# Kernel tuning notes

Hardware: AMD Instinct MI355X
Metric: run time of the kernel (lower is better)

## Reference

```python
import jax, jax.numpy as jnp
import numpy as np

B, S, D, H = 2, 48, 256, 8
DH = D // H  # depth per head = 32
N = S * S    # flattened pair sequence length = 2304


def setup_inputs() -> dict:
    key = jax.random.key(0)
    ks = jax.random.split(key, 9)
    std = 1.0 / np.sqrt(D)
    x = jax.random.normal(ks[0], (B, S, S, D), dtype=jnp.float32)
    Wq = jax.random.normal(ks[1], (D, D), dtype=jnp.float32) * std
    Wk = jax.random.normal(ks[2], (D, D), dtype=jnp.float32) * std
    Wv = jax.random.normal(ks[3], (D, D), dtype=jnp.float32) * std
    Wo = jax.random.normal(ks[4], (D, D), dtype=jnp.float32) * std
    bq = jnp.zeros((D,), jnp.float32)
    bk = jnp.zeros((D,), jnp.float32)
    bv = jnp.zeros((D,), jnp.float32)
    bo = jnp.zeros((D,), jnp.float32)
    return {"pair_representation": x, "Wq": Wq, "bq": bq, "Wk": Wk, "bk": bk,
            "Wv": Wv, "bv": bv, "Wo": Wo, "bo": bo}


def reference(pair_representation, Wq, bq, Wk, bk, Wv, bv, Wo, bo):
    x = pair_representation.reshape(B, N, D)  # flatten (S,S) -> N

    def heads(t):  # (B,N,D) -> (B,H,N,DH)
        return t.reshape(B, N, H, DH).transpose(0, 2, 1, 3)

    q = heads(x @ Wq + bq)
    k = heads(x @ Wk + bk)
    v = heads(x @ Wv + bv)

    scale = 1.0 / jnp.sqrt(jnp.asarray(DH, jnp.float32))
    logits = jnp.einsum('bhnd,bhmd->bhnm', q, k) * scale  # (B,H,N,N)
    attn = jax.nn.softmax(logits, axis=-1)
    ctx = jnp.einsum('bhnm,bhmd->bhnd', attn, v)
    ctx = ctx.transpose(0, 2, 1, 3).reshape(B, N, D)
    return ctx @ Wo + bo  # (B, N, D)
```

## Files before the change

### kernel.cpp

```cpp
#include <hip/hip_runtime.h>
#include <math.h>

#define B 2
#define S 48
#define D 256
#define H 8
#define DH 32
#define N (S*S)
#define BN (B*N)
#define BH (B*H)
#define KS 6
#define KPZ (N/KS)
#define NE ((size_t)BN*D)
#define BHN (BH*N)

typedef _Float16 half8 __attribute__((ext_vector_type(8)));
typedef _Float16 half4_t __attribute__((ext_vector_type(4)));
typedef unsigned short ushort8_t __attribute__((ext_vector_type(8)));
typedef float floatx4 __attribute__((ext_vector_type(4)));

__device__ __forceinline__ half8 cvt8(const float* v) {
    half8 h;
    #pragma unroll
    for (int j = 0; j < 8; j++) h[j] = (_Float16)v[j];
    return h;
}

__global__ __launch_bounds__(256) void proj_kernel(
    const float* __restrict__ x,
    const float* __restrict__ Wq, const float* __restrict__ bq,
    const float* __restrict__ Wk, const float* __restrict__ bk,
    const float* __restrict__ Wv, const float* __restrict__ bv,
    _Float16* __restrict__ qbuf, _Float16* __restrict__ kbuf,
    _Float16* __restrict__ vtbuf)
{
    __shared__ __align__(16) _Float16 BhS[64 * 72];

    const int z = blockIdx.z;
    const float* W    = (z == 0) ? Wq : (z == 1) ? Wk : Wv;
    const float* bias = (z == 0) ? bq : (z == 1) ? bk : bv;
    const float scale = (z == 0) ? rsqrtf((float)DH) * 1.44269504f : 1.0f;

    const int t = threadIdx.x;
    const int wv2 = t >> 6, lane = t & 63, l15 = lane & 15, quad = lane >> 4;
    const int rowb = blockIdx.x * 64;
    const int colb = blockIdx.y * 64;
    const int grow = rowb + wv2 * 16 + l15;
    floatx4 acc[4] = {{0,0,0,0},{0,0,0,0},{0,0,0,0},{0,0,0,0}};

    for (int kb0 = 0; kb0 < D; kb0 += 64) {
        __syncthreads();
        #pragma unroll
        for (int i = 0; i < 2; i++) {
            int u = i * 256 + t;
            int cc = u & 63, k0 = (u >> 6) * 8;
            float v[8];
            #pragma unroll
            for (int j = 0; j < 8; j++)
                v[j] = W[(size_t)(kb0 + k0 + j) * D + colb + cc];
            *(half8*)(BhS + cc * 72 + k0) = cvt8(v);
        }
        __syncthreads();
        #pragma unroll
        for (int ksx = 0; ksx < 2; ksx++) {
            const float* xp = x + (size_t)grow * D + kb0 + ksx * 32 + quad * 8;
            float4 x0 = *(const float4*)xp;
            float4 x1 = *(const float4*)(xp + 4);
            float v[8] = {x0.x, x0.y, x0.z, x0.w, x1.x, x1.y, x1.z, x1.w};
            half8 ah = cvt8(v);
            #pragma unroll
            for (int cg = 0; cg < 4; cg++) {
                half8 bh8 = *(const half8*)(BhS + (cg * 16 + l15) * 72 + ksx * 32 + quad * 8);
                acc[cg] = __builtin_amdgcn_mfma_f32_16x16x32_f16(ah, bh8, acc[cg], 0, 0, 0);
            }
        }
    }

    const int bb = (rowb >= N) ? 1 : 0;
    #pragma unroll
    for (int cg = 0; cg < 4; cg++) {
        int col = colb + cg * 16 + l15;
        int hh = col >> 5, dh = col & 31;
        float bs = bias[col];
        if (z < 2) {
            _Float16* op = (z == 0) ? qbuf : kbuf;
            #pragma unroll
            for (int r = 0; r < 4; r++) {
                int n = rowb + wv2 * 16 + quad * 4 + r - bb * N;
                float v = (acc[cg][r] + bs) * scale;
                op[((size_t)(bb * H + hh) * N + n) * DH + dh] = (_Float16)v;
            }
        } else {
            int n0 = rowb + wv2 * 16 + quad * 4 - bb * N;
            half4_t pk;
            #pragma unroll
            for (int r = 0; r < 4; r++) pk[r] = (_Float16)(acc[cg][r] + bs);
            *(half4_t*)(vtbuf + ((size_t)(bb * H + hh) * DH + dh) * N + n0) = pk;
        }
    }
}

__global__ __launch_bounds__(256) void attn_kernel(
    const _Float16* __restrict__ qbuf, const _Float16* __restrict__ kbuf,
    const _Float16* __restrict__ vtbuf,
    _Float16* __restrict__ ctx_part, float* __restrict__ lpart)
{
    __shared__ __align__(16) _Float16 Ks[64 * 40];
    __shared__ __align__(16) _Float16 Vt[32 * 72];

    const int t = threadIdx.x;
    const int wv2 = t >> 6, lane = t & 63, l15 = lane & 15, quad = lane >> 4;
    const int bh = blockIdx.y, kz = blockIdx.z;
    const int qbase = blockIdx.x * 128 + wv2 * 32;

    half8 bq8[2];
    #pragma unroll
    for (int qg = 0; qg < 2; qg++)
        bq8[qg] = *(const half8*)(qbuf +
            ((size_t)bh * N + qbase + qg * 16 + l15) * DH + quad * 8);

    floatx4 acc[2][2] = {{{0,0,0,0},{0,0,0,0}},{{0,0,0,0},{0,0,0,0}}};
    float lsum[2] = {0.f, 0.f};

    const int skey = t >> 2, sd0 = (t & 3) * 8;
    const int svd = t >> 3, svk = (t & 7) * 8;

    for (int it = 0; it < KPZ / 64; it++) {
        const int key0 = kz * KPZ + it * 64;
        __syncthreads();
        *(ushort8_t*)(Ks + skey * 40 + sd0) =
            *(const ushort8_t*)(kbuf + ((size_t)bh * N + key0 + skey) * DH + sd0);
        *(ushort8_t*)(Vt + svd * 72 + svk) =
            *(const ushort8_t*)(vtbuf + ((size_t)bh * DH + svd) * N + key0 + svk);
        __syncthreads();

        #pragma unroll
        for (int kg = 0; kg < 4; kg++) {
            half8 ka = *(const half8*)(Ks + (kg * 16 + l15) * 40 + quad * 8);
            half4_t va0 = *(const half4_t*)(Vt + l15 * 72 + kg * 16 + quad * 4);
            half4_t va1 = *(const half4_t*)(Vt + (16 + l15) * 72 + kg * 16 + quad * 4);
            #pragma unroll
            for (int qg = 0; qg < 2; qg++) {
                floatx4 s = {0, 0, 0, 0};
                s = __builtin_amdgcn_mfma_f32_16x16x32_f16(ka, bq8[qg], s, 0, 0, 0);
                half4_t pf;
                #pragma unroll
                for (int r = 0; r < 4; r++) {
                    float p = exp2f(s[r]);
                    lsum[qg] += p;
                    pf[r] = (_Float16)p;
                }
                acc[qg][0] = __builtin_amdgcn_mfma_f32_16x16x16f16(va0, pf, acc[qg][0], 0, 0, 0);
                acc[qg][1] = __builtin_amdgcn_mfma_f32_16x16x16f16(va1, pf, acc[qg][1], 0, 0, 0);
            }
        }
    }

    const int bb = bh >> 3, hh = bh & 7;
    #pragma unroll
    for (int qg = 0; qg < 2; qg++) {
        float ls = lsum[qg];
        ls += __shfl_xor(ls, 16);
        ls += __shfl_xor(ls, 32);
        int q = qbase + qg * 16 + l15;
        if (quad == 0) lpart[(size_t)kz * BHN + bh * N + q] = ls;
        _Float16* crow = ctx_part + (size_t)kz * NE + ((size_t)bb * N + q) * D + hh * DH;
        half4_t c0, c1;
        #pragma unroll
        for (int r = 0; r < 4; r++) {
            c0[r] = (_Float16)acc[qg][0][r];
            c1[r] = (_Float16)acc[qg][1][r];
        }
        *(half4_t*)(crow + quad * 4)      = c0;
        *(half4_t*)(crow + 16 + quad * 4) = c1;
    }
}

__global__ __launch_bounds__(256) void outproj_kernel(
    const _Float16* __restrict__ ctx_part, const float* __restrict__ lpart,
    const float* __restrict__ Wo, const float* __restrict__ bo,
    float* __restrict__ out)
{
    __shared__ __align__(16) _Float16 BhS[64 * 72];
    __shared__ float Linv[64 * 8];

    const int t = threadIdx.x;
    const int wv2 = t >> 6, lane = t & 63, l15 = lane & 15, quad = lane >> 4;
    const int rowb = blockIdx.x * 64;
    const int colb = blockIdx.y * 64;
    const int grow = rowb + wv2 * 16 + l15;

    #pragma unroll
    for (int i = 0; i < 2; i++) {
        int idx = i * 256 + t;
        int r = idx >> 3, hh = idx & 7;
        int row = rowb + r;
        int bb = (row >= N) ? 1 : 0;
        int bhn = (bb * H + hh) * N + (row - bb * N);
        float ls = 0.f;
        #pragma unroll
        for (int zz = 0; zz < KS; zz++) ls += lpart[(size_t)zz * BHN + bhn];
        Linv[idx] = 1.0f / ls;
    }

    floatx4 acc[4] = {{0,0,0,0},{0,0,0,0},{0,0,0,0},{0,0,0,0}};

    for (int kb0 = 0; kb0 < D; kb0 += 64) {
        __syncthreads();
        #pragma unroll
        for (int i = 0; i < 2; i++) {
            int u = i * 256 + t;
            int cc = u & 63, k0 = (u >> 6) * 8;
            float v[8];
            #pragma unroll
            for (int j = 0; j < 8; j++)
                v[j] = Wo[(size_t)(kb0 + k0 + j) * D + colb + cc];
            *(half8*)(BhS + cc * 72 + k0) = cvt8(v);
        }
        __syncthreads();
        #pragma unroll
        for (int ksx = 0; ksx < 2; ksx++) {
            const int kcol = kb0 + ksx * 32 + quad * 8;
            float linv = Linv[(wv2 * 16 + l15) * 8 + (kcol >> 5)];
            float v[8] = {};
            #pragma unroll
            for (int zz = 0; zz < KS; zz++) {
                half8 h = *(const half8*)(ctx_part + (size_t)zz * NE + (size_t)grow * D + kcol);
                #pragma unroll
                for (int j = 0; j < 8; j++) v[j] += (float)h[j];
            }
            #pragma unroll
            for (int j = 0; j < 8; j++) v[j] *= linv;
            half8 ah = cvt8(v);
            #pragma unroll
            for (int cg = 0; cg < 4; cg++) {
                half8 bh8 = *(const half8*)(BhS + (cg * 16 + l15) * 72 + ksx * 32 + quad * 8);
                acc[cg] = __builtin_amdgcn_mfma_f32_16x16x32_f16(ah, bh8, acc[cg], 0, 0, 0);
            }
        }
    }

    #pragma unroll
    for (int cg = 0; cg < 4; cg++) {
        int col = colb + cg * 16 + l15;
        float bs = bo[col];
        #pragma unroll
        for (int r = 0; r < 4; r++) {
            int row = rowb + wv2 * 16 + quad * 4 + r;
            out[(size_t)row * D + col] = acc[cg][r] + bs;
        }
    }
}

extern "C" void kernel_launch(void* const* d_in, const int* in_sizes, int n_in,
                              void* d_out, int out_size, void* d_ws, size_t ws_size,
                              hipStream_t stream)
{
    const float* x  = (const float*)d_in[0];
    const float* Wq = (const float*)d_in[1];
    const float* bq = (const float*)d_in[2];
    const float* Wk = (const float*)d_in[3];
    const float* bk = (const float*)d_in[4];
    const float* Wv = (const float*)d_in[5];
    const float* bv = (const float*)d_in[6];
    const float* Wo = (const float*)d_in[7];
    const float* bo = (const float*)d_in[8];
    float* out = (float*)d_out;

    _Float16* ctx_part = (_Float16*)d_ws;
    float* lpart    = (float*)(ctx_part + (size_t)KS * NE);
    _Float16* qbuf  = (_Float16*)(lpart + (size_t)KS * BHN);
    _Float16* kbuf  = qbuf + NE;
    _Float16* vtbuf = kbuf + NE;

    proj_kernel<<<dim3(BN / 64, D / 64, 3), 256, 0, stream>>>(
        x, Wq, bq, Wk, bk, Wv, bv, qbuf, kbuf, vtbuf);

    attn_kernel<<<dim3(N / 128, BH, KS), 256, 0, stream>>>(
        qbuf, kbuf, vtbuf, ctx_part, lpart);

    outproj_kernel<<<dim3(BN / 64, D / 64), 256, 0, stream>>>(
        ctx_part, lpart, Wo, bo, out);
}
```

Before: 134.3 us.

## Widen projection tiles, double attention key tile, stage reduced context in LDS

The QKV projection now computes 128 output columns per block instead of 64, so each x tile is loaded once for twice as many columns. The attention kernel stages 128 keys per iteration, halving the number of barrier pairs. The output projection is re-tiled to 32 rows by 128 columns with a 2x2 wave layout, and the split-K context reduction and normalisation are done once into shared memory instead of redundantly per wave. These changes cut redundant global loads and synchronisation, at the cost of more registers, more LDS per block and fewer blocks in flight.

```diff
diff --git a/kernel.cpp b/kernel.cpp
--- a/kernel.cpp
+++ b/kernel.cpp
@@ -34,7 +34,7 @@
     _Float16* __restrict__ qbuf, _Float16* __restrict__ kbuf,
     _Float16* __restrict__ vtbuf)
 {
-    __shared__ __align__(16) _Float16 BhS[64 * 72];
+    __shared__ __align__(16) _Float16 BhS[128 * 72];
 
     const int z = blockIdx.z;
     const float* W    = (z == 0) ? Wq : (z == 1) ? Wk : Wv;
@@ -44,16 +44,17 @@
     const int t = threadIdx.x;
     const int wv2 = t >> 6, lane = t & 63, l15 = lane & 15, quad = lane >> 4;
     const int rowb = blockIdx.x * 64;
-    const int colb = blockIdx.y * 64;
+    const int colb = blockIdx.y * 128;
     const int grow = rowb + wv2 * 16 + l15;
-    floatx4 acc[4] = {{0,0,0,0},{0,0,0,0},{0,0,0,0},{0,0,0,0}};
+    floatx4 acc[8] = {{0,0,0,0},{0,0,0,0},{0,0,0,0},{0,0,0,0},
+                      {0,0,0,0},{0,0,0,0},{0,0,0,0},{0,0,0,0}};
 
     for (int kb0 = 0; kb0 < D; kb0 += 64) {
         __syncthreads();
         #pragma unroll
-        for (int i = 0; i < 2; i++) {
+        for (int i = 0; i < 4; i++) {
             int u = i * 256 + t;
-            int cc = u & 63, k0 = (u >> 6) * 8;
+            int cc = u & 127, k0 = (u >> 7) * 8;
             float v[8];
             #pragma unroll
             for (int j = 0; j < 8; j++)
@@ -69,7 +70,7 @@
             float v[8] = {x0.x, x0.y, x0.z, x0.w, x1.x, x1.y, x1.z, x1.w};
             half8 ah = cvt8(v);
             #pragma unroll
-            for (int cg = 0; cg < 4; cg++) {
+            for (int cg = 0; cg < 8; cg++) {
                 half8 bh8 = *(const half8*)(BhS + (cg * 16 + l15) * 72 + ksx * 32 + quad * 8);
                 acc[cg] = __builtin_amdgcn_mfma_f32_16x16x32_f16(ah, bh8, acc[cg], 0, 0, 0);
             }
@@ -78,7 +79,7 @@
 
     const int bb = (rowb >= N) ? 1 : 0;
     #pragma unroll
-    for (int cg = 0; cg < 4; cg++) {
+    for (int cg = 0; cg < 8; cg++) {
         int col = colb + cg * 16 + l15;
         int hh = col >> 5, dh = col & 31;
         float bs = bias[col];
@@ -105,8 +106,8 @@
     const _Float16* __restrict__ vtbuf,
     _Float16* __restrict__ ctx_part, float* __restrict__ lpart)
 {
-    __shared__ __align__(16) _Float16 Ks[64 * 40];
-    __shared__ __align__(16) _Float16 Vt[32 * 72];
+    __shared__ __align__(16) _Float16 Ks[128 * 40];
+    __shared__ __align__(16) _Float16 Vt[32 * 136];
 
     const int t = threadIdx.x;
     const int wv2 = t >> 6, lane = t & 63, l15 = lane & 15, quad = lane >> 4;
@@ -122,23 +123,24 @@
     floatx4 acc[2][2] = {{{0,0,0,0},{0,0,0,0}},{{0,0,0,0},{0,0,0,0}}};
     float lsum[2] = {0.f, 0.f};
 
-    const int skey = t >> 2, sd0 = (t & 3) * 8;
-    const int svd = t >> 3, svk = (t & 7) * 8;
-
-    for (int it = 0; it < KPZ / 64; it++) {
-        const int key0 = kz * KPZ + it * 64;
-        __syncthreads();
-        *(ushort8_t*)(Ks + skey * 40 + sd0) =
-            *(const ushort8_t*)(kbuf + ((size_t)bh * N + key0 + skey) * DH + sd0);
-        *(ushort8_t*)(Vt + svd * 72 + svk) =
-            *(const ushort8_t*)(vtbuf + ((size_t)bh * DH + svd) * N + key0 + svk);
-        __syncthreads();
-
-        #pragma unroll
-        for (int kg = 0; kg < 4; kg++) {
+    for (int it = 0; it < KPZ / 128; it++) {
+        const int key0 = kz * KPZ + it * 128;
+        __syncthreads();
+        #pragma unroll
+        for (int i = 0; i < 2; i++) {
+            int u = i * 256 + t;
+            *(ushort8_t*)(Ks + (u >> 2) * 40 + (u & 3) * 8) =
+                *(const ushort8_t*)(kbuf + ((size_t)bh * N + key0 + (u >> 2)) * DH + (u & 3) * 8);
+            *(ushort8_t*)(Vt + (u >> 4) * 136 + (u & 15) * 8) =
+                *(const ushort8_t*)(vtbuf + ((size_t)bh * DH + (u >> 4)) * N + key0 + (u & 15) * 8);
+        }
+        __syncthreads();
+
+        #pragma unroll
+        for (int kg = 0; kg < 8; kg++) {
             half8 ka = *(const half8*)(Ks + (kg * 16 + l15) * 40 + quad * 8);
-            half4_t va0 = *(const half4_t*)(Vt + l15 * 72 + kg * 16 + quad * 4);
-            half4_t va1 = *(const half4_t*)(Vt + (16 + l15) * 72 + kg * 16 + quad * 4);
+            half4_t va0 = *(const half4_t*)(Vt + l15 * 136 + kg * 16 + quad * 4);
+            half4_t va1 = *(const half4_t*)(Vt + (16 + l15) * 136 + kg * 16 + quad * 4);
             #pragma unroll
             for (int qg = 0; qg < 2; qg++) {
                 floatx4 s = {0, 0, 0, 0};
@@ -181,36 +183,51 @@
     const float* __restrict__ Wo, const float* __restrict__ bo,
     float* __restrict__ out)
 {
-    __shared__ __align__(16) _Float16 BhS[64 * 72];
-    __shared__ float Linv[64 * 8];
+    __shared__ __align__(16) _Float16 BhS[128 * 72];
+    __shared__ __align__(16) _Float16 AsS[32 * 72];
+    __shared__ float Linv[32 * 8];
 
     const int t = threadIdx.x;
     const int wv2 = t >> 6, lane = t & 63, l15 = lane & 15, quad = lane >> 4;
-    const int rowb = blockIdx.x * 64;
-    const int colb = blockIdx.y * 64;
-    const int grow = rowb + wv2 * 16 + l15;
-
-    #pragma unroll
-    for (int i = 0; i < 2; i++) {
-        int idx = i * 256 + t;
-        int r = idx >> 3, hh = idx & 7;
+    const int wr = wv2 >> 1, wc = wv2 & 1;
+    const int rowb = blockIdx.x * 32;
+    const int colb = blockIdx.y * 128;
+
+    {
+        int r = t >> 3, hh = t & 7;
         int row = rowb + r;
         int bb = (row >= N) ? 1 : 0;
         int bhn = (bb * H + hh) * N + (row - bb * N);
         float ls = 0.f;
         #pragma unroll
         for (int zz = 0; zz < KS; zz++) ls += lpart[(size_t)zz * BHN + bhn];
-        Linv[idx] = 1.0f / ls;
+        Linv[t] = 1.0f / ls;
     }
 
     floatx4 acc[4] = {{0,0,0,0},{0,0,0,0},{0,0,0,0},{0,0,0,0}};
 
     for (int kb0 = 0; kb0 < D; kb0 += 64) {
         __syncthreads();
-        #pragma unroll
-        for (int i = 0; i < 2; i++) {
+        {
+            int r = t >> 3, k0 = (t & 7) * 8;
+            int row = rowb + r;
+            int kcol = kb0 + k0;
+            float linv = Linv[r * 8 + (kcol >> 5)];
+            float v[8] = {};
+            #pragma unroll
+            for (int zz = 0; zz < KS; zz++) {
+                half8 h = *(const half8*)(ctx_part + (size_t)zz * NE + (size_t)row * D + kcol);
+                #pragma unroll
+                for (int j = 0; j < 8; j++) v[j] += (float)h[j];
+            }
+            #pragma unroll
+            for (int j = 0; j < 8; j++) v[j] *= linv;
+            *(half8*)(AsS + r * 72 + k0) = cvt8(v);
+        }
+        #pragma unroll
+        for (int i = 0; i < 4; i++) {
             int u = i * 256 + t;
-            int cc = u & 63, k0 = (u >> 6) * 8;
+            int cc = u & 127, k0 = (u >> 7) * 8;
             float v[8];
             #pragma unroll
             for (int j = 0; j < 8; j++)
@@ -220,21 +237,10 @@
         __syncthreads();
         #pragma unroll
         for (int ksx = 0; ksx < 2; ksx++) {
-            const int kcol = kb0 + ksx * 32 + quad * 8;
-            float linv = Linv[(wv2 * 16 + l15) * 8 + (kcol >> 5)];
-            float v[8] = {};
-            #pragma unroll
-            for (int zz = 0; zz < KS; zz++) {
-                half8 h = *(const half8*)(ctx_part + (size_t)zz * NE + (size_t)grow * D + kcol);
-                #pragma unroll
-                for (int j = 0; j < 8; j++) v[j] += (float)h[j];
-            }
-            #pragma unroll
-            for (int j = 0; j < 8; j++) v[j] *= linv;
-            half8 ah = cvt8(v);
+            half8 ah = *(const half8*)(AsS + (wr * 16 + l15) * 72 + ksx * 32 + quad * 8);
             #pragma unroll
             for (int cg = 0; cg < 4; cg++) {
-                half8 bh8 = *(const half8*)(BhS + (cg * 16 + l15) * 72 + ksx * 32 + quad * 8);
+                half8 bh8 = *(const half8*)(BhS + (wc * 64 + cg * 16 + l15) * 72 + ksx * 32 + quad * 8);
                 acc[cg] = __builtin_amdgcn_mfma_f32_16x16x32_f16(ah, bh8, acc[cg], 0, 0, 0);
             }
         }
@@ -242,11 +248,11 @@
 
     #pragma unroll
     for (int cg = 0; cg < 4; cg++) {
-        int col = colb + cg * 16 + l15;
+        int col = colb + wc * 64 + cg * 16 + l15;
         float bs = bo[col];
         #pragma unroll
         for (int r = 0; r < 4; r++) {
-            int row = rowb + wv2 * 16 + quad * 4 + r;
+            int row = rowb + wr * 16 + quad * 4 + r;
             out[(size_t)row * D + col] = acc[cg][r] + bs;
         }
     }
@@ -273,12 +279,12 @@
     _Float16* kbuf  = qbuf + NE;
     _Float16* vtbuf = kbuf + NE;
 
-    proj_kernel<<<dim3(BN / 64, D / 64, 3), 256, 0, stream>>>(
+    proj_kernel<<<dim3(BN / 64, D / 128, 3), 256, 0, stream>>>(
         x, Wq, bq, Wk, bk, Wv, bv, qbuf, kbuf, vtbuf);
 
     attn_kernel<<<dim3(N / 128, BH, KS), 256, 0, stream>>>(
         qbuf, kbuf, vtbuf, ctx_part, lpart);
 
-    outproj_kernel<<<dim3(BN / 64, D / 64), 256, 0, stream>>>(
+    outproj_kernel<<<dim3(BN / 32, D / 128), 256, 0, stream>>>(
         ctx_part, lpart, Wo, bo, out);
 }
```

Measured after the change: 132.2 us. About the same (-1.6%).
